# Performance work log

Measured on AMD Instinct MI355X. Metric: run time of the kernel, lower is better.

Reference implementation:

```python
import jax, jax.numpy as jnp
import numpy as np

N_HEADS = 16
D_MODEL = 1024
D_KV = 64


def setup_inputs() -> dict:
    key = jax.random.key(0)
    ks = jax.random.split(key, 5)
    x = jax.random.normal(ks[0], (4, 2048, D_MODEL), dtype=jnp.float32)
    # per-head projections stacked: [H, D_MODEL, D_KV]
    WQ = jax.random.normal(ks[1], (N_HEADS, D_MODEL, D_KV), dtype=jnp.float32) * (D_MODEL ** -0.5)
    WK = jax.random.normal(ks[2], (N_HEADS, D_MODEL, D_KV), dtype=jnp.float32) * (D_MODEL ** -0.5)
    WV = jax.random.normal(ks[3], (N_HEADS, D_MODEL, D_KV), dtype=jnp.float32) * (D_MODEL ** -0.5)
    WO = jax.random.normal(ks[4], (N_HEADS * D_KV, D_MODEL), dtype=jnp.float32) * ((N_HEADS * D_KV) ** -0.5)
    return {"x": x, "WQ": WQ, "WK": WK, "WV": WV, "WO": WO}


def reference(x, WQ, WK, WV, WO):
    # Batched over heads instead of the original per-head Python loop.
    # q,k,v: [B, H, S, Dk]
    q = jnp.einsum('bsd,hdk->bhsk', x, WQ)
    k = jnp.einsum('bsd,hdk->bhsk', x, WK)
    v = jnp.einsum('bsd,hdk->bhsk', x, WV)
    scale = 1.0 / jnp.sqrt(jnp.asarray(q.shape[-1], q.dtype))
    scores = jnp.einsum('bhqk,bhsk->bhqs', q, k) * scale  # [B, H, S, S]
    attn = jax.nn.softmax(scores, axis=-1)
    o = jnp.einsum('bhqs,bhsk->bhqk', attn, v)            # [B, H, S, Dk]
    # concat heads along feature dim == transpose + reshape
    B, H, S, Dk = o.shape
    o = o.transpose(0, 2, 1, 3).reshape(B, S, H * Dk)
    return o @ WO
```

## Files before the change

kernel.cpp:

```cpp
#include <hip/hip_runtime.h>
#include <stdint.h>
#include <stddef.h>


typedef __attribute__((ext_vector_type(8))) short short8;
typedef __attribute__((ext_vector_type(4))) float floatx4;
typedef __attribute__((ext_vector_type(16))) float floatx16;

#define MFMA_BF16(a, b, c) __builtin_amdgcn_mfma_f32_16x16x32_bf16((a), (b), (c), 0, 0, 0)
#define MFMA32_BF16(a, b, c) __builtin_amdgcn_mfma_f32_32x32x16_bf16((a), (b), (c), 0, 0, 0)

__device__ __forceinline__ unsigned short f32_bf16(float f) {
  union { float f; unsigned u; } v; v.f = f;
  unsigned r = v.u + 0x7fffu + ((v.u >> 16) & 1u);
  return (unsigned short)(r >> 16);
}

__device__ __forceinline__ unsigned cvt_pk_bf16(float a, float b) {
  unsigned r;
  asm("v_cvt_pk_bf16_f32 %0, %1, %2" : "=v"(r) : "v"(a), "v"(b));
  return r;
}

__device__ __forceinline__ float fast_exp2(float x) {
#if __has_builtin(__builtin_amdgcn_exp2f)
  return __builtin_amdgcn_exp2f(x);
#else
  return exp2f(x);
#endif
}

__device__ __forceinline__ void g2l16(const void* g, void* l) {
  __builtin_amdgcn_global_load_lds((const __attribute__((address_space(1))) void*)g,
                                   (__attribute__((address_space(3))) void*)l,
                                   16, 0, 0);
}


__global__ __launch_bounds__(256) void cvt_x_k(const float* __restrict__ x,
                                               unsigned short* __restrict__ xb) {
  int i = (blockIdx.x * 256 + threadIdx.x) * 4;
  float4 v = *(const float4*)(x + i);
  ushort4 o;
  o.x = f32_bf16(v.x); o.y = f32_bf16(v.y); o.z = f32_bf16(v.z); o.w = f32_bf16(v.w);
  *(ushort4*)(xb + i) = o;
}

__global__ __launch_bounds__(256) void cvt_w_k(const float* __restrict__ WQ,
                                               const float* __restrict__ WK,
                                               const float* __restrict__ WV,
                                               const float* __restrict__ WO,
                                               unsigned short* __restrict__ Wqkv,
                                               unsigned short* __restrict__ WOt) {
  __shared__ unsigned short tile[64][72];
  const int bid = blockIdx.x;
  const int tid = threadIdx.x;
  if (bid < 768) {
    const int th = bid >> 4;
    const int typ = th >> 4, h = th & 15;
    const float* W = (typ == 0) ? WQ : ((typ == 1) ? WK : WV);
    const float* src = W + ((size_t)h * 1024 + (bid & 15) * 64) * 64;
    #pragma unroll
    for (int it = 0; it < 16; ++it) {
      int f = it * 256 + tid;
      int dk = f & 63, dl = f >> 6;
      tile[dk][dl] = f32_bf16(src[(size_t)dl * 64 + dk]);
    }
    __syncthreads();
    unsigned short* dst = Wqkv + (size_t)(typ * 1024 + h * 64) * 1024 + (bid & 15) * 64;
    #pragma unroll
    for (int it = 0; it < 16; ++it) {
      int f = it * 256 + tid;
      int d = f & 63, dk = f >> 6;
      dst[(size_t)dk * 1024 + d] = tile[dk][d];
    }
  } else {
    const int id2 = bid - 768;
    const int nt = (id2 & 15) * 64, kt = (id2 >> 4) * 64;
    #pragma unroll
    for (int it = 0; it < 16; ++it) {
      int f = it * 256 + tid;
      int n = f & 63, kl = f >> 6;
      tile[n][kl] = f32_bf16(WO[(size_t)(kt + kl) * 1024 + nt + n]);
    }
    __syncthreads();
    #pragma unroll
    for (int it = 0; it < 16; ++it) {
      int f = it * 256 + tid;
      int k = f & 63, nl = f >> 6;
      WOt[(size_t)(nt + nl) * 1024 + kt + k] = tile[nl][k];
    }
  }
}


__global__ __launch_bounds__(256, 2)
void gemm_qkv_k(const unsigned short* __restrict__ A,
                const unsigned short* __restrict__ Bt,
                unsigned short* __restrict__ Qo,
                unsigned short* __restrict__ Ko,
                unsigned short* __restrict__ Vo) {
  __shared__ __align__(16) unsigned short As[8192];
  __shared__ __align__(16) unsigned short Bs[8192];
  const int lane = threadIdx.x & 63;
  const int wave = threadIdx.x >> 6;
  const int h32 = lane >> 5;
  const int c32 = lane & 31;
  const int wm = wave >> 1, wn = wave & 1;
  const int row0 = blockIdx.y * 128;
  const int col0 = blockIdx.x * 128;

  floatx16 acc[2][2];
  #pragma unroll
  for (int i = 0; i < 2; ++i)
    #pragma unroll
    for (int j = 0; j < 2; ++j) acc[i][j] = (floatx16)0.0f;

  for (int k0 = 0; k0 < 1024; k0 += 64) {
    #pragma unroll
    for (int i = 0; i < 4; ++i) {
      int s = (wave * 4 + i) * 64 + lane;
      int r = s >> 3, kc = (s & 7) ^ (r & 7);
      g2l16(A  + (size_t)(row0 + r) * 1024 + k0 + kc * 8, As + (wave * 4 + i) * 512);
      g2l16(Bt + (size_t)(col0 + r) * 1024 + k0 + kc * 8, Bs + (wave * 4 + i) * 512);
    }
    __syncthreads();
    #pragma unroll
    for (int dc = 0; dc < 4; ++dc) {
      short8 af[2], bf[2];
      #pragma unroll
      for (int mi = 0; mi < 2; ++mi) {
        int r = wm * 64 + mi * 32 + c32;
        int g = (dc * 2 + h32) ^ (r & 7);
        af[mi] = *(const short8*)(As + (r * 8 + g) * 8);
      }
      #pragma unroll
      for (int ni = 0; ni < 2; ++ni) {
        int r = wn * 64 + ni * 32 + c32;
        int g = (dc * 2 + h32) ^ (r & 7);
        bf[ni] = *(const short8*)(Bs + (r * 8 + g) * 8);
      }
      #pragma unroll
      for (int mi = 0; mi < 2; ++mi)
        #pragma unroll
        for (int ni = 0; ni < 2; ++ni)
          acc[mi][ni] = MFMA32_BF16(af[mi], bf[ni], acc[mi][ni]);
    }
    __syncthreads();
  }

  const int typ = col0 >> 10;
  const float qscale = 0.18033688011112042f;
  #pragma unroll
  for (int mi = 0; mi < 2; ++mi) {
    #pragma unroll
    for (int gg = 0; gg < 4; ++gg) {
      int grow0 = row0 + wm * 64 + mi * 32 + 8 * gg + 4 * h32;
      int b = grow0 >> 11;
      int s = grow0 & 2047;
      int quad16 = (2 * gg + h32) & 3;
      int qp = ((quad16 & 1) << 1) | (quad16 >> 1);
      #pragma unroll
      for (int ni = 0; ni < 2; ++ni) {
        int gcol = col0 + wn * 64 + ni * 32 + c32;
        int rem = gcol & 1023;
        int h = rem >> 6, dk = rem & 63;
        int bhh = b * 16 + h;
        if (typ == 0) {
          #pragma unroll
          for (int rr = 0; rr < 4; ++rr)
            Qo[((size_t)bhh * 2048 + s + rr) * 64 + dk] = f32_bf16(acc[mi][ni][gg * 4 + rr] * qscale);
        } else if (typ == 1) {
          #pragma unroll
          for (int rr = 0; rr < 4; ++rr)
            Ko[((size_t)bhh * 2048 + s + rr) * 64 + dk] = f32_bf16(acc[mi][ni][gg * 4 + rr]);
        } else {
          ushort4 pv;
          pv.x = f32_bf16(acc[mi][ni][gg * 4 + 0]);
          pv.y = f32_bf16(acc[mi][ni][gg * 4 + 1]);
          pv.z = f32_bf16(acc[mi][ni][gg * 4 + 2]);
          pv.w = f32_bf16(acc[mi][ni][gg * 4 + 3]);
          int sp = (s & ~15) | (qp << 2);
          *(ushort4*)(Vo + ((size_t)bhh * 64 + dk) * 2048 + sp) = pv;
        }
      }
    }
  }
}


__global__ __launch_bounds__(256, 2)
void attn_k(const unsigned short* __restrict__ Qg_,
            const unsigned short* __restrict__ Kg_,
            const unsigned short* __restrict__ Vg_,
            unsigned short* __restrict__ O) {
  __shared__ __align__(16) char smem[65536];
  const int lane = threadIdx.x & 63;
  const int wave = threadIdx.x >> 6;
  const int h32 = lane >> 5;
  const int c32 = lane & 31;
  const int bh = blockIdx.x;
  const int q0 = blockIdx.y * 256;
  const unsigned short* Qg = Qg_ + ((size_t)bh * 2048 + q0) * 64;
  const unsigned short* Kg = Kg_ + (size_t)bh * 2048 * 64;
  const unsigned short* Vg = Vg_ + (size_t)bh * 64 * 2048;

  short8 qf[2][4];
  #pragma unroll
  for (int g = 0; g < 2; ++g) {
    int rq = wave * 64 + g * 32 + c32;
    #pragma unroll
    for (int dc = 0; dc < 4; ++dc)
      qf[g][dc] = *(const short8*)(Qg + (size_t)rq * 64 + dc * 16 + h32 * 8);
  }

  union { unsigned u[4]; short8 s8; } onesf;
  #pragma unroll
  for (int i = 0; i < 4; ++i) onesf.u[i] = 0x3F803F80u;

  floatx16 acc[2][2], accs[2];
  #pragma unroll
  for (int g = 0; g < 2; ++g) {
    acc[g][0] = (floatx16)0.0f; acc[g][1] = (floatx16)0.0f; accs[g] = (floatx16)0.0f;
  }

  auto stage = [&](int s0, int boff) {
    #pragma unroll
    for (int i = 0; i < 4; ++i) {
      int s = (wave * 4 + i) * 64 + lane;
      int rk = s >> 3, ck = (s & 7) ^ (rk & 7);
      g2l16(Kg + (size_t)(s0 + rk) * 64 + ck * 8, smem + boff + s * 16);
      int rv = s >> 4, cv = (s & 15) ^ (rv & 7);
      g2l16(Vg + (size_t)rv * 2048 + s0 + cv * 8, smem + boff + 16384 + s * 16);
    }
  };

  stage(0, 0);
  asm volatile("s_waitcnt vmcnt(0)\ns_barrier" ::: "memory");

  for (int it = 0; it < 16; ++it) {
    const int boff = (it & 1) << 15;
    if (it < 15) {
      stage((it + 1) * 128, boff ^ 32768);
      asm volatile("s_waitcnt vmcnt(8)\ns_barrier" ::: "memory");
    } else {
      asm volatile("s_waitcnt vmcnt(0)\ns_barrier" ::: "memory");
    }
    const char* kbase = smem + boff;
    const char* vbase = smem + boff + 16384;

    #pragma unroll
    for (int kb = 0; kb < 4; ++kb) {
      floatx16 sc0 = (floatx16)0.0f, sc1 = (floatx16)0.0f;
      __builtin_amdgcn_s_setprio(1);
      #pragma unroll
      for (int dc = 0; dc < 4; ++dc) {
        int rk = kb * 32 + c32;
        int kc = (dc * 2 + h32) ^ (rk & 7);
        short8 kf = *(const short8*)(kbase + (rk * 8 + kc) * 16);
        sc0 = MFMA32_BF16(kf, qf[0][dc], sc0);
        sc1 = MFMA32_BF16(kf, qf[1][dc], sc1);
      }
      __builtin_amdgcn_s_setprio(0);
      unsigned pk0[8], pk1[8];
      #pragma unroll
      for (int i = 0; i < 8; ++i) {
        float a0 = fast_exp2(sc0[2 * i]), b0 = fast_exp2(sc0[2 * i + 1]);
        float a1 = fast_exp2(sc1[2 * i]), b1 = fast_exp2(sc1[2 * i + 1]);
        pk0[i] = cvt_pk_bf16(a0, b0);
        pk1[i] = cvt_pk_bf16(a1, b1);
      }
      __builtin_amdgcn_s_setprio(1);
      #pragma unroll
      for (int st = 0; st < 2; ++st) {
        union { unsigned u[4]; short8 s8; } af0, af1;
        #pragma unroll
        for (int i = 0; i < 4; ++i) { af0.u[i] = pk0[4 * st + i]; af1.u[i] = pk1[4 * st + i]; }
        int cc = kb * 4 + st * 2 + h32;
        #pragma unroll
        for (int nb = 0; nb < 2; ++nb) {
          int rv = nb * 32 + c32;
          short8 bv = *(const short8*)(vbase + (rv * 16 + (cc ^ (rv & 7))) * 16);
          acc[0][nb] = MFMA32_BF16(af0.s8, bv, acc[0][nb]);
          acc[1][nb] = MFMA32_BF16(af1.s8, bv, acc[1][nb]);
        }
        accs[0] = MFMA32_BF16(af0.s8, onesf.s8, accs[0]);
        accs[1] = MFMA32_BF16(af1.s8, onesf.s8, accs[1]);
      }
      __builtin_amdgcn_s_setprio(0);
    }
    asm volatile("s_barrier" ::: "memory");
  }

  const int b = bh >> 4, h = bh & 15;
  #pragma unroll
  for (int g = 0; g < 2; ++g) {
    #pragma unroll
    for (int gg = 0; gg < 4; ++gg) {
      #pragma unroll
      for (int rr = 0; rr < 4; ++rr) {
        int qrel = rr + 8 * gg + 4 * h32;
        float rl = 1.0f / accs[g][4 * gg + rr];
        int token = b * 2048 + q0 + wave * 64 + g * 32 + qrel;
        size_t base = (size_t)token * 1024 + h * 64;
        O[base + c32]      = f32_bf16(acc[g][0][4 * gg + rr] * rl);
        O[base + 32 + c32] = f32_bf16(acc[g][1][4 * gg + rr] * rl);
      }
    }
  }
}


__global__ __launch_bounds__(256, 2)
void gemm_out_k(const unsigned short* __restrict__ A,
                const unsigned short* __restrict__ Bt,
                float* __restrict__ C) {
  __shared__ __align__(16) unsigned short As[8192];
  __shared__ __align__(16) unsigned short Bs[8192];
  const int lane = threadIdx.x & 63;
  const int wave = threadIdx.x >> 6;
  const int h32 = lane >> 5;
  const int c32 = lane & 31;
  const int wm = wave >> 1, wn = wave & 1;
  const int row0 = blockIdx.y * 128;
  const int col0 = blockIdx.x * 128;

  floatx16 acc[2][2];
  #pragma unroll
  for (int i = 0; i < 2; ++i)
    #pragma unroll
    for (int j = 0; j < 2; ++j) acc[i][j] = (floatx16)0.0f;

  for (int k0 = 0; k0 < 1024; k0 += 64) {
    #pragma unroll
    for (int i = 0; i < 4; ++i) {
      int s = (wave * 4 + i) * 64 + lane;
      int r = s >> 3, kc = (s & 7) ^ (r & 7);
      g2l16(A  + (size_t)(row0 + r) * 1024 + k0 + kc * 8, As + (wave * 4 + i) * 512);
      g2l16(Bt + (size_t)(col0 + r) * 1024 + k0 + kc * 8, Bs + (wave * 4 + i) * 512);
    }
    __syncthreads();
    #pragma unroll
    for (int dc = 0; dc < 4; ++dc) {
      short8 af[2], bf[2];
      #pragma unroll
      for (int mi = 0; mi < 2; ++mi) {
        int r = wm * 64 + mi * 32 + c32;
        int g = (dc * 2 + h32) ^ (r & 7);
        af[mi] = *(const short8*)(As + (r * 8 + g) * 8);
      }
      #pragma unroll
      for (int ni = 0; ni < 2; ++ni) {
        int r = wn * 64 + ni * 32 + c32;
        int g = (dc * 2 + h32) ^ (r & 7);
        bf[ni] = *(const short8*)(Bs + (r * 8 + g) * 8);
      }
      #pragma unroll
      for (int mi = 0; mi < 2; ++mi)
        #pragma unroll
        for (int ni = 0; ni < 2; ++ni)
          acc[mi][ni] = MFMA32_BF16(af[mi], bf[ni], acc[mi][ni]);
    }
    __syncthreads();
  }

  #pragma unroll
  for (int mi = 0; mi < 2; ++mi) {
    #pragma unroll
    for (int ni = 0; ni < 2; ++ni) {
      #pragma unroll
      for (int gg = 0; gg < 4; ++gg) {
        #pragma unroll
        for (int rr = 0; rr < 4; ++rr) {
          int row = row0 + wm * 64 + mi * 32 + rr + 8 * gg + 4 * h32;
          int col = col0 + wn * 64 + ni * 32 + c32;
          C[(size_t)row * 1024 + col] = acc[mi][ni][gg * 4 + rr];
        }
      }
    }
  }
}


extern "C" void kernel_launch(void* const* d_in, const int* in_sizes, int n_in,
                              void* d_out, int out_size, void* d_ws, size_t ws_size,
                              hipStream_t stream) {
  const float* x  = (const float*)d_in[0];
  const float* WQ = (const float*)d_in[1];
  const float* WK = (const float*)d_in[2];
  const float* WV = (const float*)d_in[3];
  const float* WO = (const float*)d_in[4];
  char* ws = (char*)d_ws;
  unsigned short* xb   = (unsigned short*)(ws);
  unsigned short* Wqkv = (unsigned short*)(ws + (size_t)16 * 1024 * 1024);
  unsigned short* WOt  = (unsigned short*)(ws + (size_t)22 * 1024 * 1024);
  unsigned short* Qb   = (unsigned short*)(ws + (size_t)24 * 1024 * 1024);
  unsigned short* Kb   = (unsigned short*)(ws + (size_t)40 * 1024 * 1024);
  unsigned short* Vb   = (unsigned short*)(ws + (size_t)56 * 1024 * 1024);
  float* out = (float*)d_out;

  cvt_x_k<<<8192, 256, 0, stream>>>(x, xb);
  cvt_w_k<<<1024, 256, 0, stream>>>(WQ, WK, WV, WO, Wqkv, WOt);
  gemm_qkv_k<<<dim3(24, 64), 256, 0, stream>>>(xb, Wqkv, Qb, Kb, Vb);
  attn_k<<<dim3(64, 8), 256, 0, stream>>>(Qb, Kb, Vb, xb );
  gemm_out_k<<<dim3(8, 64), 256, 0, stream>>>(xb, WOt, out);
}
```

Before: 255.6 us.

## Double-buffer LDS tiles in QKV and output GEMMs to overlap loads with MFMA

Both projection GEMMs now keep two LDS buffers for A and B. The next K-tile is prefetched with direct global-to-LDS loads while MFMAs run on the current tile, synchronised by partial vmcnt waits and raw barriers. Wave priority is raised during the MFMA section. This aims to hide global memory latency inside the GEMM main loops. LDS use doubles to 64KB per block, which may limit occupancy at 2 blocks per CU.

Result: slower. 263.7 us (+3.2%).

```diff
diff --git a/kernel.cpp b/kernel.cpp
--- a/kernel.cpp
+++ b/kernel.cpp
@@ -100,8 +100,8 @@
                 unsigned short* __restrict__ Qo,
                 unsigned short* __restrict__ Ko,
                 unsigned short* __restrict__ Vo) {
-  __shared__ __align__(16) unsigned short As[8192];
-  __shared__ __align__(16) unsigned short Bs[8192];
+  __shared__ __align__(16) unsigned short As[2][8192];
+  __shared__ __align__(16) unsigned short Bs[2][8192];
   const int lane = threadIdx.x & 63;
   const int wave = threadIdx.x >> 6;
   const int h32 = lane >> 5;
@@ -116,15 +116,28 @@
     #pragma unroll
     for (int j = 0; j < 2; ++j) acc[i][j] = (floatx16)0.0f;
 
-  for (int k0 = 0; k0 < 1024; k0 += 64) {
+  auto stage = [&](int k0, int p) {
     #pragma unroll
     for (int i = 0; i < 4; ++i) {
       int s = (wave * 4 + i) * 64 + lane;
       int r = s >> 3, kc = (s & 7) ^ (r & 7);
-      g2l16(A  + (size_t)(row0 + r) * 1024 + k0 + kc * 8, As + (wave * 4 + i) * 512);
-      g2l16(Bt + (size_t)(col0 + r) * 1024 + k0 + kc * 8, Bs + (wave * 4 + i) * 512);
-    }
-    __syncthreads();
+      g2l16(A  + (size_t)(row0 + r) * 1024 + k0 + kc * 8, As[p] + (wave * 4 + i) * 512);
+      g2l16(Bt + (size_t)(col0 + r) * 1024 + k0 + kc * 8, Bs[p] + (wave * 4 + i) * 512);
+    }
+  };
+
+  stage(0, 0);
+  asm volatile("s_waitcnt vmcnt(0)\ns_barrier" ::: "memory");
+
+  for (int kt = 0; kt < 16; ++kt) {
+    const int p = kt & 1;
+    if (kt < 15) {
+      stage((kt + 1) * 64, p ^ 1);
+      asm volatile("s_waitcnt vmcnt(8)\ns_barrier" ::: "memory");
+    } else {
+      asm volatile("s_waitcnt vmcnt(0)\ns_barrier" ::: "memory");
+    }
+    __builtin_amdgcn_s_setprio(1);
     #pragma unroll
     for (int dc = 0; dc < 4; ++dc) {
       short8 af[2], bf[2];
@@ -132,13 +145,13 @@
       for (int mi = 0; mi < 2; ++mi) {
         int r = wm * 64 + mi * 32 + c32;
         int g = (dc * 2 + h32) ^ (r & 7);
-        af[mi] = *(const short8*)(As + (r * 8 + g) * 8);
+        af[mi] = *(const short8*)(As[p] + (r * 8 + g) * 8);
       }
       #pragma unroll
       for (int ni = 0; ni < 2; ++ni) {
         int r = wn * 64 + ni * 32 + c32;
         int g = (dc * 2 + h32) ^ (r & 7);
-        bf[ni] = *(const short8*)(Bs + (r * 8 + g) * 8);
+        bf[ni] = *(const short8*)(Bs[p] + (r * 8 + g) * 8);
       }
       #pragma unroll
       for (int mi = 0; mi < 2; ++mi)
@@ -146,7 +159,8 @@
         for (int ni = 0; ni < 2; ++ni)
           acc[mi][ni] = MFMA32_BF16(af[mi], bf[ni], acc[mi][ni]);
     }
-    __syncthreads();
+    __builtin_amdgcn_s_setprio(0);
+    asm volatile("s_barrier" ::: "memory");
   }
 
   const int typ = col0 >> 10;
@@ -315,8 +329,8 @@
 void gemm_out_k(const unsigned short* __restrict__ A,
                 const unsigned short* __restrict__ Bt,
                 float* __restrict__ C) {
-  __shared__ __align__(16) unsigned short As[8192];
-  __shared__ __align__(16) unsigned short Bs[8192];
+  __shared__ __align__(16) unsigned short As[2][8192];
+  __shared__ __align__(16) unsigned short Bs[2][8192];
   const int lane = threadIdx.x & 63;
   const int wave = threadIdx.x >> 6;
   const int h32 = lane >> 5;
@@ -331,15 +345,28 @@
     #pragma unroll
     for (int j = 0; j < 2; ++j) acc[i][j] = (floatx16)0.0f;
 
-  for (int k0 = 0; k0 < 1024; k0 += 64) {
+  auto stage = [&](int k0, int p) {
     #pragma unroll
     for (int i = 0; i < 4; ++i) {
       int s = (wave * 4 + i) * 64 + lane;
       int r = s >> 3, kc = (s & 7) ^ (r & 7);
-      g2l16(A  + (size_t)(row0 + r) * 1024 + k0 + kc * 8, As + (wave * 4 + i) * 512);
-      g2l16(Bt + (size_t)(col0 + r) * 1024 + k0 + kc * 8, Bs + (wave * 4 + i) * 512);
-    }
-    __syncthreads();
+      g2l16(A  + (size_t)(row0 + r) * 1024 + k0 + kc * 8, As[p] + (wave * 4 + i) * 512);
+      g2l16(Bt + (size_t)(col0 + r) * 1024 + k0 + kc * 8, Bs[p] + (wave * 4 + i) * 512);
+    }
+  };
+
+  stage(0, 0);
+  asm volatile("s_waitcnt vmcnt(0)\ns_barrier" ::: "memory");
+
+  for (int kt = 0; kt < 16; ++kt) {
+    const int p = kt & 1;
+    if (kt < 15) {
+      stage((kt + 1) * 64, p ^ 1);
+      asm volatile("s_waitcnt vmcnt(8)\ns_barrier" ::: "memory");
+    } else {
+      asm volatile("s_waitcnt vmcnt(0)\ns_barrier" ::: "memory");
+    }
+    __builtin_amdgcn_s_setprio(1);
     #pragma unroll
     for (int dc = 0; dc < 4; ++dc) {
       short8 af[2], bf[2];
@@ -347,13 +374,13 @@
       for (int mi = 0; mi < 2; ++mi) {
         int r = wm * 64 + mi * 32 + c32;
         int g = (dc * 2 + h32) ^ (r & 7);
-        af[mi] = *(const short8*)(As + (r * 8 + g) * 8);
+        af[mi] = *(const short8*)(As[p] + (r * 8 + g) * 8);
       }
       #pragma unroll
       for (int ni = 0; ni < 2; ++ni) {
         int r = wn * 64 + ni * 32 + c32;
         int g = (dc * 2 + h32) ^ (r & 7);
-        bf[ni] = *(const short8*)(Bs + (r * 8 + g) * 8);
+        bf[ni] = *(const short8*)(Bs[p] + (r * 8 + g) * 8);
       }
       #pragma unroll
       for (int mi = 0; mi < 2; ++mi)
@@ -361,7 +388,8 @@
         for (int ni = 0; ni < 2; ++ni)
           acc[mi][ni] = MFMA32_BF16(af[mi], bf[ni], acc[mi][ni]);
     }
-    __syncthreads();
+    __builtin_amdgcn_s_setprio(0);
+    asm volatile("s_barrier" ::: "memory");
   }
 
   #pragma unroll
```
